# Kernel tuning notes

Measured on AMD Instinct MI355X. Metric: run time of the kernel, lower is better.

The kernel has to match this reference:

```python
import jax, jax.numpy as jnp
import numpy as np

B, L, K, D = 16, 2048, 24, 64  # batch, seq_len (input_len), num_eigh, d_out (= d_in)


def _hankel_eigh(l, k):
    # Hankel matrix Z[i,j] = 2 / ((i+j)^3 - (i+j)), 1-indexed (spectral filtering of LDS)
    s = np.arange(1, l + 1, dtype=np.int64)[:, None] + np.arange(1, l + 1, dtype=np.int64)[None, :]
    z = 2.0 / (s.astype(np.float64) ** 3 - s.astype(np.float64))
    ev, evec = np.linalg.eigh(z)
    # top-k eigenpairs (eigh returns ascending order)
    return jnp.asarray(ev[-k:], jnp.float32), jnp.asarray(evec[:, -k:], jnp.float32)


def setup_inputs() -> dict:
    key = jax.random.key(0)
    k1, k2 = jax.random.split(key)
    inputs = jax.random.normal(k1, (B, L, D), dtype=jnp.float32)
    m_phi = jax.random.normal(k2, (D * K, D), dtype=jnp.float32) / np.float32(np.sqrt(D * K))
    eig_vals, eig_vecs = _hankel_eigh(L, K)  # [K], [L, K]
    return {"inputs": inputs, "m_phi": m_phi, "eig_vals": eig_vals, "eig_vecs": eig_vecs}


def _compute_x_tilde(inputs, eig_vals, eig_vecs):
    # Causal FFT convolution of each Hankel eigenvector (filter, length L) with input.
    l = inputs.shape[1]
    n = 2 * l  # fft length >= 2l - 1 for linear (non-circular) convolution
    V = jnp.fft.rfft(eig_vecs, n=n, axis=0)            # [F, K]
    U = jnp.fft.rfft(inputs, n=n, axis=1)              # [B, F, D]
    prod = V[None, :, :, None] * U[:, :, None, :]      # [B, F, K, D]
    x = jnp.fft.irfft(prod, n=n, axis=1)[:, :l]        # truncate to causal part: [B, L, K, D]
    x = x * (eig_vals ** 0.25)[None, None, :, None]    # spectral scaling
    return x.reshape(x.shape[0], l, -1)                # [B, L, K*D]


def reference(inputs, m_phi, eig_vals, eig_vecs):
    x_tilde = _compute_x_tilde(inputs, eig_vals, eig_vecs)
    return x_tilde @ m_phi  # delta_phi: [B, L, D]
```

## Files before the change

kernel.cpp:

```cpp
#include <hip/hip_runtime.h>

typedef _Float16 f16;
typedef _Float16 f16x4 __attribute__((ext_vector_type(4)));
typedef _Float16 f16x8 __attribute__((ext_vector_type(8)));
typedef float f32x4 __attribute__((ext_vector_type(4)));

__device__ __forceinline__ void gl_lds16(const void* g, void* l) {
  __builtin_amdgcn_global_load_lds(
      (__attribute__((address_space(1))) unsigned int*)(g),
      (__attribute__((address_space(3))) unsigned int*)(l), 16, 0, 0);
}

__global__ __launch_bounds__(256) void k_pre0(const float* __restrict__ in,
                                              const float* __restrict__ m_phi,
                                              const float* __restrict__ ev,
                                              const float* __restrict__ evec,
                                              f16* __restrict__ phiT,
                                              f16* __restrict__ uin,
                                              f16* __restrict__ Dpre,
                                              float* __restrict__ out) {
  __shared__ float esm[256];
  int blk = blockIdx.x;
  int tid = threadIdx.x;
  if (blk < 256) {
    int b = blk >> 4, s0 = (blk & 15) * 128;
    f16* up = uin + (size_t)blk * 8192;
#pragma unroll
    for (int v = 0; v < 4; ++v) {
      int flat = v * 256 + tid;
      int row = flat >> 3, cl = flat & 7, cg = cl ^ (row & 7);
      const float* g = in + ((size_t)(b * 2048 + s0 + row)) * 64 + cg * 8;
      float4 u0 = *(const float4*)g;
      float4 u1 = *(const float4*)(g + 4);
      f16x8 h;
      h[0] = (f16)u0.x; h[1] = (f16)u0.y; h[2] = (f16)u0.z; h[3] = (f16)u0.w;
      h[4] = (f16)u1.x; h[5] = (f16)u1.y; h[6] = (f16)u1.z; h[7] = (f16)u1.w;
      *(f16x8*)&up[flat * 8] = h;
    }
    return;
  }
  if (blk < 280) {
    int k = blk - 256;
    for (int idx = tid; idx < 4096; idx += 256) {
      int e = idx >> 6, d = idx & 63;
      phiT[k * 4096 + idx] = (f16)m_phi[(k * 64 + d) * 64 + e];
    }
    return;
  }
  if (blk < 664) {
    int a = blk - 280;
    int diag = a / 24, k = a % 24;
    float s4 = sqrtf(sqrtf(ev[k]));
    int base = diag * 128 - 127;
    if (tid < 255) {
      int v = base + tid;
      esm[tid] = (v >= 0) ? evec[v * 24 + k] * s4 : 0.0f;
    }
    __syncthreads();
    f16* plane = Dpre + (size_t)(diag * 24 + k) * 2560;
    for (int i = tid; i < 2560; i += 256) {
      float val = 0.f;
      if (i < 2112) {
        int p = i / 264, y = i - p * 264;
        int g = 254 - p - y;
        if (g >= 0) val = esm[g];
      }
      plane[i] = (f16)val;
    }
    return;
  }
  float4* o = (float4*)(out + (size_t)(blk - 664) * 32768);
  float4 z4 = {0.f, 0.f, 0.f, 0.f};
#pragma unroll
  for (int i = 0; i < 32; ++i) o[i * 256 + tid] = z4;
}

__global__ __launch_bounds__(256) void k_w(const f16* __restrict__ uin,
                                           const f16* __restrict__ phiT,
                                           f16* __restrict__ W2T) {
  __shared__ __align__(16) f16 Ubuf[8320];
  __shared__ __align__(16) f16 Psm[64 * 64];
  int wblk = blockIdx.x;
  int s0 = (wblk & 15) * 128;
  int b = (wblk >> 4) & 15;
  int kg = wblk >> 8;
  int tid = threadIdx.x, lane = tid & 63, wv = tid >> 6;
  const f16* up = uin + (size_t)(wblk & 255) * 8192;
#pragma unroll
  for (int v = 0; v < 4; ++v)
    gl_lds16(up + (size_t)(v * 256 + tid) * 8, &Ubuf[(v * 256 + wv * 64) * 8]);
  {
    int k0 = kg * 4;
#pragma unroll
    for (int v = 0; v < 2; ++v) {
      int flat = v * 256 + tid;
      int row = flat >> 3, cl = flat & 7, cg = cl ^ (row & 7);
      gl_lds16(phiT + (size_t)k0 * 4096 + row * 64 + cg * 8,
               &Psm[(v * 256 + wv * 64) * 8]);
    }
  }
  __syncthreads();
  int wm = wv * 32;
  f16x8 af[2][2];
#pragma unroll
  for (int ks = 0; ks < 2; ++ks)
#pragma unroll
    for (int x = 0; x < 2; ++x) {
      int m = wm + x * 16 + (lane & 15);
      int ch = (ks * 4 + (lane >> 4)) ^ (m & 7);
      af[ks][x] = *(const f16x8*)&Ubuf[m * 64 + ch * 8];
    }
  for (int ki = 0; ki < 4; ++ki) {
    int k = kg * 4 + ki;
    f32x4 zero = {0.f, 0.f, 0.f, 0.f};
    f32x4 acc[2][4];
#pragma unroll
    for (int x = 0; x < 2; ++x)
#pragma unroll
      for (int y = 0; y < 4; ++y) acc[x][y] = zero;
#pragma unroll
    for (int ks = 0; ks < 2; ++ks) {
      f16x8 bf[4];
#pragma unroll
      for (int y = 0; y < 4; ++y) {
        int n = y * 16 + (lane & 15);
        int ch = (ks * 4 + (lane >> 4)) ^ (n & 7);
        bf[y] = *(const f16x8*)&Psm[n * 64 + ch * 8];
      }
#pragma unroll
      for (int x = 0; x < 2; ++x)
#pragma unroll
        for (int y = 0; y < 4; ++y)
          acc[x][y] = __builtin_amdgcn_mfma_f32_16x16x32_f16(af[ks][x], bf[y], acc[x][y], 0, 0, 0);
    }
    __syncthreads();
#pragma unroll
    for (int x = 0; x < 2; ++x)
#pragma unroll
      for (int y = 0; y < 4; ++y) {
        int e = y * 16 + (lane & 15);
        int sg = wm + x * 16 + ((lane >> 4) << 2);
        f16x4 pk;
        pk[0] = (f16)acc[x][y][0]; pk[1] = (f16)acc[x][y][1];
        pk[2] = (f16)acc[x][y][2]; pk[3] = (f16)acc[x][y][3];
        *(f16x4*)&Ubuf[e * 130 + sg] = pk;
      }
    if (ki < 3) {
      int kn = k + 1;
#pragma unroll
      for (int v = 0; v < 2; ++v) {
        int flat = v * 256 + tid;
        int row = flat >> 3, cl = flat & 7, cg = cl ^ (row & 7);
        gl_lds16(phiT + (size_t)kn * 4096 + row * 64 + cg * 8,
                 &Psm[(v * 256 + wv * 64) * 8]);
      }
    }
    __syncthreads();
#pragma unroll
    for (int pass = 0; pass < 4; ++pass) {
      int g = pass * 256 + tid;
      int e = g >> 4, ch = g & 15;
      f16x8 val = *(const f16x8*)&Ubuf[e * 130 + ch * 8];
      *(f16x8*)&W2T[((size_t)((b * 24 + k) * 64 + e)) * 2048 + s0 + ch * 8] = val;
    }
  }
}

__global__ __launch_bounds__(256, 3) void k_main(const f16* __restrict__ Dpre,
                                                 const f16* __restrict__ W2T,
                                                 float* __restrict__ out) {
  __shared__ __align__(16) f16 Bsm[128 * 128];
  __shared__ __align__(16) f16 Dsm[2560];
  int nt = blockIdx.x;
  int q = blockIdx.y;
  int diag = 0, off = 0;
  while (off + (16 - diag) <= q) { off += 16 - diag; ++diag; }
  int st = q - off;
  int mt = st + diag;
  int tid = threadIdx.x, lane = tid & 63, wv = tid >> 6;
  int wm = (wv & 1) * 64, wn = (wv >> 1) * 64;
  int b0 = nt * 2;
  int ml = lane & 15, qv = lane >> 4;
  int p264 = (7 - (ml & 7)) * 264;
  int yb = (ml < 8 ? 120 : 112) - wm;

  f32x4 zero = {0.f, 0.f, 0.f, 0.f};
  f32x4 acc[4][4];
#pragma unroll
  for (int x = 0; x < 4; ++x)
#pragma unroll
    for (int y = 0; y < 4; ++y) acc[x][y] = zero;

  const f16* dplane = Dpre + (size_t)(diag * 24) * 2560;

  for (int k = 0; k < 24; ++k) {
    const f16* dk = dplane + k * 2560;
    gl_lds16(dk + tid * 8, &Dsm[(wv * 64) * 8]);
    if (wv == 0) gl_lds16(dk + (256 + lane) * 8, &Dsm[2048]);
#pragma unroll
    for (int v = 0; v < 8; ++v) {
      int flat = v * 256 + tid;
      int row = flat >> 4, cl = flat & 15, cg = cl ^ (row & 15);
      int bb = b0 + (row >> 6), e = row & 63;
      gl_lds16(W2T + ((size_t)((bb * 24 + k) * 64 + e)) * 2048 + st * 128 + cg * 8,
               &Bsm[(v * 256 + wv * 64) * 8]);
    }
    __syncthreads();
#pragma unroll
    for (int ks = 0; ks < 4; ++ks) {
      int s0q = ks * 32 + qv * 8;
      f16x8 af[4], bf[4];
#pragma unroll
      for (int x = 0; x < 4; ++x)
        af[x] = *(const f16x8*)&Dsm[p264 + s0q - x * 16 + yb];
#pragma unroll
      for (int y = 0; y < 4; ++y) {
        int n = wn + y * 16 + ml;
        int cl = (ks * 4 + qv) ^ (n & 15);
        bf[y] = *(const f16x8*)&Bsm[n * 128 + cl * 8];
      }
#pragma unroll
      for (int x = 0; x < 4; ++x)
#pragma unroll
        for (int y = 0; y < 4; ++y)
          acc[x][y] = __builtin_amdgcn_mfma_f32_16x16x32_f16(af[x], bf[y], acc[x][y], 0, 0, 0);
    }
    __syncthreads();
  }
  int t0 = mt * 128 + wm;
  int n0 = nt * 128 + wn;
#pragma unroll
  for (int x = 0; x < 4; ++x) {
    int rbase = t0 + x * 16 + (qv << 2);
#pragma unroll
    for (int y = 0; y < 4; ++y) {
      int col = n0 + y * 16 + ml;
      int b = col >> 6, e = col & 63;
#pragma unroll
      for (int r = 0; r < 4; ++r)
        atomicAdd(&out[((size_t)(b * 2048 + rbase + r)) * 64 + e], acc[x][y][r]);
    }
  }
}

extern "C" void kernel_launch(void* const* d_in, const int* in_sizes, int n_in,
                              void* d_out, int out_size, void* d_ws, size_t ws_size,
                              hipStream_t stream) {
  const float* inputs = (const float*)d_in[0];
  const float* m_phi = (const float*)d_in[1];
  const float* ev = (const float*)d_in[2];
  const float* evec = (const float*)d_in[3];
  float* out = (float*)d_out;
  char* ws = (char*)d_ws;
  f16* Dpre = (f16*)(ws);
  f16* phiT = (f16*)(ws + 1966080);
  f16* uin = (f16*)(ws + 2162688);
  f16* W2T = (f16*)(ws + 6356992);

  hipLaunchKernelGGL(k_pre0, dim3(728), dim3(256), 0, stream,
                     inputs, m_phi, ev, evec, phiT, uin, Dpre, out);
  hipLaunchKernelGGL(k_w, dim3(1536), dim3(256), 0, stream, uin, phiT, W2T);
  hipLaunchKernelGGL(k_main, dim3(8, 136), dim3(256), 0, stream, Dpre, W2T, out);
}
```

Baseline: 210.2 us.

## Double-buffer LDS tiles in main GEMM loop to overlap loads with MFMA

Splits the shared-memory B and D tiles into two buffers and issues the asynchronous global-to-LDS loads for step k+1 before computing step k. Partial vmcnt waits let the compute start as soon as the current tile has landed, and s_setprio raises wave priority during the MFMA section. The aim is to hide global load latency behind matrix math. The cost is double the LDS footprint, so occupancy drops from 3 to 2 blocks per CU, and the hand-counted vmcnt values are fragile if the compiler reorders or splits the loads.

```diff
diff --git a/kernel.cpp b/kernel.cpp
--- a/kernel.cpp
+++ b/kernel.cpp
@@ -166,11 +166,11 @@
   }
 }
 
-__global__ __launch_bounds__(256, 3) void k_main(const f16* __restrict__ Dpre,
+__global__ __launch_bounds__(256, 2) void k_main(const f16* __restrict__ Dpre,
                                                  const f16* __restrict__ W2T,
                                                  float* __restrict__ out) {
-  __shared__ __align__(16) f16 Bsm[128 * 128];
-  __shared__ __align__(16) f16 Dsm[2560];
+  __shared__ __align__(16) f16 Bsm[2][128 * 128];
+  __shared__ __align__(16) f16 Dsm[2][2560];
   int nt = blockIdx.x;
   int q = blockIdx.y;
   int diag = 0, off = 0;
@@ -193,31 +193,50 @@
 
   const f16* dplane = Dpre + (size_t)(diag * 24) * 2560;
 
-  for (int k = 0; k < 24; ++k) {
-    const f16* dk = dplane + k * 2560;
-    gl_lds16(dk + tid * 8, &Dsm[(wv * 64) * 8]);
-    if (wv == 0) gl_lds16(dk + (256 + lane) * 8, &Dsm[2048]);
+  auto stage = [&](int buf, int kk) {
+    const f16* dk = dplane + kk * 2560;
+    gl_lds16(dk + tid * 8, &Dsm[buf][wv * 512]);
+    if (wv == 0) gl_lds16(dk + (256 + lane) * 8, &Dsm[buf][2048]);
 #pragma unroll
     for (int v = 0; v < 8; ++v) {
       int flat = v * 256 + tid;
       int row = flat >> 4, cl = flat & 15, cg = cl ^ (row & 15);
       int bb = b0 + (row >> 6), e = row & 63;
-      gl_lds16(W2T + ((size_t)((bb * 24 + k) * 64 + e)) * 2048 + st * 128 + cg * 8,
-               &Bsm[(v * 256 + wv * 64) * 8]);
-    }
-    __syncthreads();
+      gl_lds16(W2T + ((size_t)((bb * 24 + kk) * 64 + e)) * 2048 + st * 128 + cg * 8,
+               &Bsm[buf][(v * 256 + wv * 64) * 8]);
+    }
+  };
+
+  stage(0, 0);
+
+#pragma unroll 2
+  for (int k = 0; k < 24; ++k) {
+    const int cur = k & 1;
+    if (k < 23) {
+      stage(cur ^ 1, k + 1);
+      __builtin_amdgcn_sched_barrier(0);
+      if (wv == 0)
+        asm volatile("s_waitcnt vmcnt(10)" ::: "memory");
+      else
+        asm volatile("s_waitcnt vmcnt(9)" ::: "memory");
+    } else {
+      asm volatile("s_waitcnt vmcnt(0)" ::: "memory");
+    }
+    __builtin_amdgcn_s_barrier();
+    __builtin_amdgcn_sched_barrier(0);
+    __builtin_amdgcn_s_setprio(1);
 #pragma unroll
     for (int ks = 0; ks < 4; ++ks) {
       int s0q = ks * 32 + qv * 8;
       f16x8 af[4], bf[4];
 #pragma unroll
       for (int x = 0; x < 4; ++x)
-        af[x] = *(const f16x8*)&Dsm[p264 + s0q - x * 16 + yb];
+        af[x] = *(const f16x8*)&Dsm[cur][p264 + s0q - x * 16 + yb];
 #pragma unroll
       for (int y = 0; y < 4; ++y) {
         int n = wn + y * 16 + ml;
         int cl = (ks * 4 + qv) ^ (n & 15);
-        bf[y] = *(const f16x8*)&Bsm[n * 128 + cl * 8];
+        bf[y] = *(const f16x8*)&Bsm[cur][n * 128 + cl * 8];
       }
 #pragma unroll
       for (int x = 0; x < 4; ++x)
@@ -225,8 +244,13 @@
         for (int y = 0; y < 4; ++y)
           acc[x][y] = __builtin_amdgcn_mfma_f32_16x16x32_f16(af[x], bf[y], acc[x][y], 0, 0, 0);
     }
-    __syncthreads();
-  }
+    __builtin_amdgcn_s_setprio(0);
+    __builtin_amdgcn_sched_barrier(0);
+    asm volatile("" ::: "memory");
+    __builtin_amdgcn_s_barrier();
+    asm volatile("" ::: "memory");
+  }
+
   int t0 = mt * 128 + wm;
   int n0 = nt * 128 + wn;
 #pragma unroll
```

Result: slower. 233.4 us (+11.1%).

## Compute two diagonal output tiles per block to reuse the W2T B-tile

Applied to the files above, without the earlier changes.

Each k_main block now handles two adjacent diagonals (Toeplitz tiles) sharing the same source tile st, so the 128x128 W2T tile loaded into LDS feeds two sets of MFMAs. The grid shrinks from 136 to 72 blocks per column, which cuts global B-tile traffic roughly in half. The cost is doubled accumulator registers (32 f32x4 per thread), which may reduce occupancy below the declared 3 blocks per CU or cause spills. Fewer blocks also means fewer waves available to hide latency, and some blocks get uneven work when a diagonal has no partner.

```diff
diff --git a/kernel.cpp b/kernel.cpp
--- a/kernel.cpp
+++ b/kernel.cpp
@@ -170,13 +170,16 @@
                                                  const f16* __restrict__ W2T,
                                                  float* __restrict__ out) {
   __shared__ __align__(16) f16 Bsm[128 * 128];
-  __shared__ __align__(16) f16 Dsm[2560];
+  __shared__ __align__(16) f16 Dsm[2][2560];
   int nt = blockIdx.x;
-  int q = blockIdx.y;
-  int diag = 0, off = 0;
-  while (off + (16 - diag) <= q) { off += 16 - diag; ++diag; }
-  int st = q - off;
-  int mt = st + diag;
+  int p = blockIdx.y;
+  int st = 0, off = 0;
+  while (off + ((17 - st) >> 1) <= p) { off += (17 - st) >> 1; ++st; }
+  int dp = p - off;
+  int diag0 = dp * 2;
+  int has2 = (diag0 + 1 <= 15 - st);
+  int diag1 = has2 ? diag0 + 1 : diag0;
+  int mt0 = st + diag0, mt1 = st + diag1;
   int tid = threadIdx.x, lane = tid & 63, wv = tid >> 6;
   int wm = (wv & 1) * 64, wn = (wv >> 1) * 64;
   int b0 = nt * 2;
@@ -185,18 +188,27 @@
   int yb = (ml < 8 ? 120 : 112) - wm;
 
   f32x4 zero = {0.f, 0.f, 0.f, 0.f};
-  f32x4 acc[4][4];
-#pragma unroll
-  for (int x = 0; x < 4; ++x)
-#pragma unroll
-    for (int y = 0; y < 4; ++y) acc[x][y] = zero;
-
-  const f16* dplane = Dpre + (size_t)(diag * 24) * 2560;
-
+  f32x4 acc[2][4][4];
+#pragma unroll
+  for (int t = 0; t < 2; ++t)
+#pragma unroll
+    for (int x = 0; x < 4; ++x)
+#pragma unroll
+      for (int y = 0; y < 4; ++y) acc[t][x][y] = zero;
+
+  const f16* dpl0 = Dpre + (size_t)(diag0 * 24) * 2560;
+  const f16* dpl1 = Dpre + (size_t)(diag1 * 24) * 2560;
+
+#pragma unroll 1
   for (int k = 0; k < 24; ++k) {
-    const f16* dk = dplane + k * 2560;
-    gl_lds16(dk + tid * 8, &Dsm[(wv * 64) * 8]);
-    if (wv == 0) gl_lds16(dk + (256 + lane) * 8, &Dsm[2048]);
+    const f16* dk0 = dpl0 + k * 2560;
+    const f16* dk1 = dpl1 + k * 2560;
+    gl_lds16(dk0 + tid * 8, &Dsm[0][wv * 512]);
+    gl_lds16(dk1 + tid * 8, &Dsm[1][wv * 512]);
+    if (wv == 0) {
+      gl_lds16(dk0 + (256 + lane) * 8, &Dsm[0][2048]);
+      gl_lds16(dk1 + (256 + lane) * 8, &Dsm[1][2048]);
+    }
 #pragma unroll
     for (int v = 0; v < 8; ++v) {
       int flat = v * 256 + tid;
@@ -209,10 +221,7 @@
 #pragma unroll
     for (int ks = 0; ks < 4; ++ks) {
       int s0q = ks * 32 + qv * 8;
-      f16x8 af[4], bf[4];
-#pragma unroll
-      for (int x = 0; x < 4; ++x)
-        af[x] = *(const f16x8*)&Dsm[p264 + s0q - x * 16 + yb];
+      f16x8 bf[4];
 #pragma unroll
       for (int y = 0; y < 4; ++y) {
         int n = wn + y * 16 + ml;
@@ -220,25 +229,39 @@
         bf[y] = *(const f16x8*)&Bsm[n * 128 + cl * 8];
       }
 #pragma unroll
-      for (int x = 0; x < 4; ++x)
-#pragma unroll
-        for (int y = 0; y < 4; ++y)
-          acc[x][y] = __builtin_amdgcn_mfma_f32_16x16x32_f16(af[x], bf[y], acc[x][y], 0, 0, 0);
-    }
-    __syncthreads();
-  }
-  int t0 = mt * 128 + wm;
+      for (int t = 0; t < 2; ++t) {
+        f16x8 af[4];
+#pragma unroll
+        for (int x = 0; x < 4; ++x)
+          af[x] = *(const f16x8*)&Dsm[t][p264 + s0q - x * 16 + yb];
+#pragma unroll
+        for (int x = 0; x < 4; ++x)
+#pragma unroll
+          for (int y = 0; y < 4; ++y)
+            acc[t][x][y] = __builtin_amdgcn_mfma_f32_16x16x32_f16(
+                af[x], bf[y], acc[t][x][y], 0, 0, 0);
+      }
+    }
+    __syncthreads();
+  }
+
   int n0 = nt * 128 + wn;
 #pragma unroll
-  for (int x = 0; x < 4; ++x) {
-    int rbase = t0 + x * 16 + (qv << 2);
-#pragma unroll
-    for (int y = 0; y < 4; ++y) {
-      int col = n0 + y * 16 + ml;
-      int b = col >> 6, e = col & 63;
-#pragma unroll
-      for (int r = 0; r < 4; ++r)
-        atomicAdd(&out[((size_t)(b * 2048 + rbase + r)) * 64 + e], acc[x][y][r]);
+  for (int t = 0; t < 2; ++t) {
+    if (t == 1 && !has2) break;
+    int t0 = (t ? mt1 : mt0) * 128 + wm;
+#pragma unroll
+    for (int x = 0; x < 4; ++x) {
+      int rbase = t0 + x * 16 + (qv << 2);
+#pragma unroll
+      for (int y = 0; y < 4; ++y) {
+        int col = n0 + y * 16 + ml;
+        int b = col >> 6, e = col & 63;
+#pragma unroll
+        for (int r = 0; r < 4; ++r)
+          atomicAdd(&out[((size_t)(b * 2048 + rbase + r)) * 64 + e],
+                    acc[t][x][y][r]);
+      }
     }
   }
 }
@@ -260,5 +283,5 @@
   hipLaunchKernelGGL(k_pre0, dim3(728), dim3(256), 0, stream,
                      inputs, m_phi, ev, evec, phiT, uin, Dpre, out);
   hipLaunchKernelGGL(k_w, dim3(1536), dim3(256), 0, stream, uin, phiT, W2T);
-  hipLaunchKernelGGL(k_main, dim3(8, 136), dim3(256), 0, stream, Dpre, W2T, out);
-}
+  hipLaunchKernelGGL(k_main, dim3(8, 72), dim3(256), 0, stream, Dpre, W2T, out);
+}
```

After: 317.8 us. 51.2% more time.

## Retile Toeplitz GEMM to 256-wide time tiles per batch with sliding A-fragment reuse

Applied to the files above, without the earlier changes.

The main Toeplitz-conv GEMM switches from 128x128 tiles over two batches to 256-row time tiles over one batch's 64 channels. Because each Toeplitz tile is constant along its diagonals, adjacent A fragments are reused by shifting a register window, so only one new A fragment is loaded per k-step. The precomputed diagonal planes are enlarged to match the wider tiles. This cuts grid blocks and atomics and reduces LDS reads per MFMA. The trade-off is more accumulator registers per wave and fewer blocks (576 versus 1088), which may hurt occupancy or load balance.

```diff
diff --git a/kernel.cpp b/kernel.cpp
--- a/kernel.cpp
+++ b/kernel.cpp
@@ -19,7 +19,7 @@
                                               f16* __restrict__ uin,
                                               f16* __restrict__ Dpre,
                                               float* __restrict__ out) {
-  __shared__ float esm[256];
+  __shared__ float esm[512];
   int blk = blockIdx.x;
   int tid = threadIdx.x;
   if (blk < 256) {
@@ -47,29 +47,34 @@
     }
     return;
   }
-  if (blk < 664) {
+  if (blk < 472) {
     int a = blk - 280;
     int diag = a / 24, k = a % 24;
     float s4 = sqrtf(sqrtf(ev[k]));
-    int base = diag * 128 - 127;
-    if (tid < 255) {
-      int v = base + tid;
-      esm[tid] = (v >= 0) ? evec[v * 24 + k] * s4 : 0.0f;
-    }
-    __syncthreads();
-    f16* plane = Dpre + (size_t)(diag * 24 + k) * 2560;
-    for (int i = tid; i < 2560; i += 256) {
+    int base = diag * 256 - 255;
+    {
+      int v0 = base + tid;
+      esm[tid] = (v0 >= 0) ? evec[v0 * 24 + k] * s4 : 0.0f;
+      if (tid < 255) {
+        int v1 = base + 256 + tid;
+        esm[256 + tid] = (v1 >= 0) ? evec[v1 * 24 + k] * s4 : 0.0f;
+      }
+      if (tid == 255) esm[511] = 0.0f;
+    }
+    __syncthreads();
+    f16* plane = Dpre + (size_t)(diag * 24 + k) * 4608;
+    for (int i = tid; i < 4608; i += 256) {
       float val = 0.f;
-      if (i < 2112) {
-        int p = i / 264, y = i - p * 264;
-        int g = 254 - p - y;
+      if (i < 4160) {
+        int p = i / 520, y = i - p * 520;
+        int g = 510 - p - y;
         if (g >= 0) val = esm[g];
       }
       plane[i] = (f16)val;
     }
     return;
   }
-  float4* o = (float4*)(out + (size_t)(blk - 664) * 32768);
+  float4* o = (float4*)(out + (size_t)(blk - 472) * 32768);
   float4 z4 = {0.f, 0.f, 0.f, 0.f};
 #pragma unroll
   for (int i = 0; i < 32; ++i) o[i * 256 + tid] = z4;
@@ -169,76 +174,84 @@
 __global__ __launch_bounds__(256, 3) void k_main(const f16* __restrict__ Dpre,
                                                  const f16* __restrict__ W2T,
                                                  float* __restrict__ out) {
-  __shared__ __align__(16) f16 Bsm[128 * 128];
-  __shared__ __align__(16) f16 Dsm[2560];
-  int nt = blockIdx.x;
-  int q = blockIdx.y;
-  int diag = 0, off = 0;
-  while (off + (16 - diag) <= q) { off += 16 - diag; ++diag; }
-  int st = q - off;
+  __shared__ __align__(16) f16 Bsm[64 * 256];
+  __shared__ __align__(16) f16 Dsm[4608];
+  int q = blockIdx.x;
+  int b = blockIdx.y;
+  int st = 0, off = 0;
+  while (off + (8 - st) <= q) { off += 8 - st; ++st; }
+  int diag = q - off;
   int mt = st + diag;
   int tid = threadIdx.x, lane = tid & 63, wv = tid >> 6;
-  int wm = (wv & 1) * 64, wn = (wv >> 1) * 64;
-  int b0 = nt * 2;
+  int wm2 = (wv & 1) * 16;
+  int wn = (wv >> 1) * 32;
   int ml = lane & 15, qv = lane >> 4;
-  int p264 = (7 - (ml & 7)) * 264;
-  int yb = (ml < 8 ? 120 : 112) - wm;
+  int p520 = (7 - (ml & 7)) * 520;
+  int yb2 = (ml < 8 ? 120 : 112) - wm2;
+  int dbase = p520 + yb2 + qv * 8 + 128;
 
   f32x4 zero = {0.f, 0.f, 0.f, 0.f};
-  f32x4 acc[4][4];
-#pragma unroll
-  for (int x = 0; x < 4; ++x)
-#pragma unroll
-    for (int y = 0; y < 4; ++y) acc[x][y] = zero;
-
-  const f16* dplane = Dpre + (size_t)(diag * 24) * 2560;
-
+  f32x4 acc[8][2];
+#pragma unroll
+  for (int x = 0; x < 8; ++x)
+#pragma unroll
+    for (int y = 0; y < 2; ++y) acc[x][y] = zero;
+
+  const f16* dpl = Dpre + (size_t)(diag * 24) * 4608;
+
+#pragma unroll 1
   for (int k = 0; k < 24; ++k) {
-    const f16* dk = dplane + k * 2560;
-    gl_lds16(dk + tid * 8, &Dsm[(wv * 64) * 8]);
-    if (wv == 0) gl_lds16(dk + (256 + lane) * 8, &Dsm[2048]);
+    const f16* dk = dpl + (size_t)k * 4608;
+    gl_lds16(dk + (size_t)tid * 8, &Dsm[(wv * 64) * 8]);
+    gl_lds16(dk + (size_t)(256 + tid) * 8, &Dsm[(256 + wv * 64) * 8]);
+    if (wv == 0) gl_lds16(dk + (size_t)(512 + lane) * 8, &Dsm[512 * 8]);
 #pragma unroll
     for (int v = 0; v < 8; ++v) {
       int flat = v * 256 + tid;
-      int row = flat >> 4, cl = flat & 15, cg = cl ^ (row & 15);
-      int bb = b0 + (row >> 6), e = row & 63;
-      gl_lds16(W2T + ((size_t)((bb * 24 + k) * 64 + e)) * 2048 + st * 128 + cg * 8,
+      int row = flat >> 5, cl = flat & 31, cg = cl ^ (row & 31);
+      gl_lds16(W2T + ((size_t)((b * 24 + k) * 64 + row)) * 2048 + st * 256 + cg * 8,
                &Bsm[(v * 256 + wv * 64) * 8]);
     }
     __syncthreads();
-#pragma unroll
-    for (int ks = 0; ks < 4; ++ks) {
-      int s0q = ks * 32 + qv * 8;
-      f16x8 af[4], bf[4];
-#pragma unroll
-      for (int x = 0; x < 4; ++x)
-        af[x] = *(const f16x8*)&Dsm[p264 + s0q - x * 16 + yb];
-#pragma unroll
-      for (int y = 0; y < 4; ++y) {
+    f16x8 w[8];
+#pragma unroll
+    for (int j = 0; j < 8; ++j)
+      w[j] = *(const f16x8*)&Dsm[dbase + 32 * (j - 7)];
+#pragma unroll
+    for (int ks = 0; ks < 8; ++ks) {
+      if (ks > 0) {
+#pragma unroll
+        for (int j = 0; j < 7; ++j) w[j] = w[j + 1];
+        w[7] = *(const f16x8*)&Dsm[dbase + 32 * ks];
+      }
+      f16x8 bf[2];
+#pragma unroll
+      for (int y = 0; y < 2; ++y) {
         int n = wn + y * 16 + ml;
-        int cl = (ks * 4 + qv) ^ (n & 15);
-        bf[y] = *(const f16x8*)&Bsm[n * 128 + cl * 8];
-      }
-#pragma unroll
-      for (int x = 0; x < 4; ++x)
-#pragma unroll
-        for (int y = 0; y < 4; ++y)
-          acc[x][y] = __builtin_amdgcn_mfma_f32_16x16x32_f16(af[x], bf[y], acc[x][y], 0, 0, 0);
-    }
-    __syncthreads();
-  }
-  int t0 = mt * 128 + wm;
-  int n0 = nt * 128 + wn;
-#pragma unroll
-  for (int x = 0; x < 4; ++x) {
-    int rbase = t0 + x * 16 + (qv << 2);
-#pragma unroll
-    for (int y = 0; y < 4; ++y) {
-      int col = n0 + y * 16 + ml;
-      int b = col >> 6, e = col & 63;
+        int cl = (ks * 4 + qv) ^ (n & 31);
+        bf[y] = *(const f16x8*)&Bsm[n * 256 + cl * 8];
+      }
+#pragma unroll
+      for (int x = 0; x < 8; ++x)
+#pragma unroll
+        for (int y = 0; y < 2; ++y)
+          acc[x][y] = __builtin_amdgcn_mfma_f32_16x16x32_f16(
+              w[7 - x], bf[y], acc[x][y], 0, 0, 0);
+    }
+    __syncthreads();
+  }
+
+  int t0 = mt * 256 + wm2;
+#pragma unroll
+  for (int x = 0; x < 8; ++x) {
+    int rbase = t0 + x * 32 + (qv << 2);
+#pragma unroll
+    for (int y = 0; y < 2; ++y) {
+      int e = wn + y * 16 + ml;
 #pragma unroll
       for (int r = 0; r < 4; ++r)
-        atomicAdd(&out[((size_t)(b * 2048 + rbase + r)) * 64 + e], acc[x][y][r]);
+        atomicAdd(&out[((size_t)(b * 2048 + rbase + r)) * 64 + e],
+                  acc[x][y][r]);
     }
   }
 }
@@ -257,8 +270,8 @@
   f16* uin = (f16*)(ws + 2162688);
   f16* W2T = (f16*)(ws + 6356992);
 
-  hipLaunchKernelGGL(k_pre0, dim3(728), dim3(256), 0, stream,
+  hipLaunchKernelGGL(k_pre0, dim3(536), dim3(256), 0, stream,
                      inputs, m_phi, ev, evec, phiT, uin, Dpre, out);
   hipLaunchKernelGGL(k_w, dim3(1536), dim3(256), 0, stream, uin, phiT, W2T);
-  hipLaunchKernelGGL(k_main, dim3(8, 136), dim3(256), 0, stream, Dpre, W2T, out);
-}
+  hipLaunchKernelGGL(k_main, dim3(36, 16), dim3(256), 0, stream, Dpre, W2T, out);
+}
```

New measurement: 234.8 us. 11.7% more time.
